# Performance work log

Hardware: AMD Instinct MI355X
Metric: run time of the kernel (lower is better)

The kernel has to match this reference:

```python
import jax, jax.numpy as jnp
import numpy as np

N = 262144          # number of samples
D = 512             # embedding dim
NUM_IDS = 8192      # label vocabulary size (fixed segment count for jit)


def setup_inputs() -> dict:
    key = jax.random.key(0)
    k_emb, k_lab = jax.random.split(key)
    emb = jax.random.normal(k_emb, (N, D), dtype=jnp.float32)
    labels = jax.random.randint(k_lab, (N,), 0, NUM_IDS, dtype=jnp.int64)
    return {"emb": emb, "labels": labels}


def reference(emb, labels):
    # torch.unique(labels, return_inverse=True); fixed size for jit.
    uniq_ids, inv = jnp.unique(labels, return_inverse=True, size=NUM_IDS, fill_value=-1)
    # scatter_add_ of rows grouped by inverse index -> segmented sum
    summed = jax.ops.segment_sum(emb, inv, num_segments=NUM_IDS)   # [NUM_IDS, D]
    # bincount(inv, minlength=num_ids)
    counts = jnp.bincount(inv, length=NUM_IDS)                      # [NUM_IDS]
    agg = summed / jnp.maximum(counts, 1).astype(emb.dtype)[:, None]
    return (agg, uniq_ids)
```

## Files before the change

### kernel.cpp

```cpp
#include <hip/hip_runtime.h>

#define NUM_IDS 8192
#define D 512


__global__ __launch_bounds__(256) void k_zero(int* __restrict__ cnt, int* __restrict__ cursor) {
    int i = blockIdx.x * 256 + threadIdx.x;
    if (i < NUM_IDS) { cnt[i] = 0; cursor[i] = 0; }
}

__global__ __launch_bounds__(256) void k_count(const int* __restrict__ labels, int n,
                                               int* __restrict__ cnt) {
    int i = blockIdx.x * 256 + threadIdx.x;
    if (i < n) atomicAdd(&cnt[labels[i]], 1);
}

__global__ __launch_bounds__(1024) void k_scan(const int* __restrict__ cnt,
                                               int* __restrict__ rank,
                                               int* __restrict__ offs,
                                               int* __restrict__ nuniq,
                                               float* __restrict__ uniq_out) {
    __shared__ int s_f[16], s_c[16];
    __shared__ int s_total;
    int t = threadIdx.x;
    int lane = t & 63, wave = t >> 6;
    int c[8], f[8];
    int fs = 0, cs = 0;
    int base = t * 8;
#pragma unroll
    for (int j = 0; j < 8; ++j) {
        c[j] = cnt[base + j];
        f[j] = (c[j] > 0) ? 1 : 0;
        fs += f[j]; cs += c[j];
    }
    int fi = fs, ci = cs;
#pragma unroll
    for (int d = 1; d < 64; d <<= 1) {
        int fo = __shfl_up(fi, d, 64);
        int co = __shfl_up(ci, d, 64);
        if (lane >= d) { fi += fo; ci += co; }
    }
    if (lane == 63) { s_f[wave] = fi; s_c[wave] = ci; }
    __syncthreads();
    if (t == 0) {
        int af = 0, ac = 0;
#pragma unroll
        for (int w = 0; w < 16; ++w) {
            int tf = s_f[w], tc = s_c[w];
            s_f[w] = af; s_c[w] = ac;
            af += tf; ac += tc;
        }
        s_total = af;
        nuniq[0] = af;
    }
    __syncthreads();
    int fexcl = (fi - fs) + s_f[wave];
    int cexcl = (ci - cs) + s_c[wave];
    int total = s_total;
#pragma unroll
    for (int j = 0; j < 8; ++j) {
        int id = base + j;
        rank[id] = fexcl;
        offs[id] = cexcl;
        if (f[j]) uniq_out[fexcl] = (float)id;
        if (id >= total) uniq_out[id] = -1.0f;
        fexcl += f[j];
        cexcl += c[j];
    }
}

__global__ __launch_bounds__(256) void k_fill(const int* __restrict__ labels, int n,
                                              const int* __restrict__ offs,
                                              int* __restrict__ cursor,
                                              int* __restrict__ rowidx) {
    int i = blockIdx.x * 256 + threadIdx.x;
    if (i < n) {
        int id = labels[i];
        int p = atomicAdd(&cursor[id], 1);
        rowidx[offs[id] + p] = i;
    }
}

__global__ __launch_bounds__(128) void k_agg(const float* __restrict__ emb,
                                             const int* __restrict__ cnt,
                                             const int* __restrict__ rank,
                                             const int* __restrict__ offs,
                                             const int* __restrict__ rowidx,
                                             const int* __restrict__ nuniq,
                                             float* __restrict__ agg) {
    int id = blockIdx.x;
    int t = threadIdx.x;
    int n = cnt[id];
    if (n == 0) {
        int outrow = nuniq[0] + (id - rank[id]);
        float4 z = {0.f, 0.f, 0.f, 0.f};
        reinterpret_cast<float4*>(agg + (size_t)outrow * D)[t] = z;
        return;
    }
    int off = offs[id];
    float ax0 = 0.f, ay0 = 0.f, az0 = 0.f, aw0 = 0.f;
    float ax1 = 0.f, ay1 = 0.f, az1 = 0.f, aw1 = 0.f;
    int r = 0;
    for (; r + 2 <= n; r += 2) {
        int r0 = rowidx[off + r];
        int r1 = rowidx[off + r + 1];
        float4 v0 = reinterpret_cast<const float4*>(emb + (size_t)r0 * D)[t];
        float4 v1 = reinterpret_cast<const float4*>(emb + (size_t)r1 * D)[t];
        ax0 += v0.x; ay0 += v0.y; az0 += v0.z; aw0 += v0.w;
        ax1 += v1.x; ay1 += v1.y; az1 += v1.z; aw1 += v1.w;
    }
    if (r < n) {
        int r0 = rowidx[off + r];
        float4 v0 = reinterpret_cast<const float4*>(emb + (size_t)r0 * D)[t];
        ax0 += v0.x; ay0 += v0.y; az0 += v0.z; aw0 += v0.w;
    }
    float inv = 1.0f / (float)n;
    float4 o;
    o.x = (ax0 + ax1) * inv;
    o.y = (ay0 + ay1) * inv;
    o.z = (az0 + az1) * inv;
    o.w = (aw0 + aw1) * inv;
    reinterpret_cast<float4*>(agg + (size_t)rank[id] * D)[t] = o;
}


extern "C" void kernel_launch(void* const* d_in, const int* in_sizes, int n_in,
                              void* d_out, int out_size, void* d_ws, size_t ws_size,
                              hipStream_t stream) {
    const float* emb   = (const float*)d_in[0];
    const int* labels  = (const int*)d_in[1];
    const int n = in_sizes[1];

    float* agg  = (float*)d_out;
    float* uniq = agg + (size_t)NUM_IDS * D;

    int* ws     = (int*)d_ws;
    int* cnt    = ws;
    int* rank   = ws + NUM_IDS;
    int* offs   = ws + 2 * NUM_IDS;
    int* cursor = ws + 3 * NUM_IDS;
    int* nuniq  = ws + 4 * NUM_IDS;
    int* rowidx = ws + 4 * NUM_IDS + 64;

    k_zero <<<NUM_IDS / 256, 256, 0, stream>>>(cnt, cursor);
    k_count<<<(n + 255) / 256, 256, 0, stream>>>(labels, n, cnt);
    k_scan <<<1, 1024, 0, stream>>>(cnt, rank, offs, nuniq, uniq);
    k_fill <<<(n + 255) / 256, 256, 0, stream>>>(labels, n, offs, cursor, rowidx);
    k_agg  <<<NUM_IDS, 128, 0, stream>>>(emb, cnt, rank, offs, rowidx, nuniq, agg);
}
```

Before: 155.3 us.

## Fuse count and scan via last-block ticket, preload cursor offsets, unroll aggregation

Merges the label counting and the prefix scan into one kernel. The last block to finish, detected through an atomic ticket, performs the scan with 256 threads over 32 ids each. Zeroing moves to a memset, and the cursor is seeded with the segment offsets so the fill step needs one atomic and no offs lookup. The aggregation loop is unrolled to four rows in flight per iteration. This removes two kernel launches and the serial single-block scan launch, in exchange for a grid-wide fence and a smaller scan block.

```diff
diff --git a/kernel.cpp b/kernel.cpp
--- a/kernel.cpp
+++ b/kernel.cpp
@@ -4,34 +4,39 @@
 #define D 512
 
 
-__global__ __launch_bounds__(256) void k_zero(int* __restrict__ cnt, int* __restrict__ cursor) {
-    int i = blockIdx.x * 256 + threadIdx.x;
-    if (i < NUM_IDS) { cnt[i] = 0; cursor[i] = 0; }
-}
+__global__ __launch_bounds__(256) void k_count_scan(
+    const int* __restrict__ labels, int n,
+    int* __restrict__ cnt,
+    int* __restrict__ rank,
+    int* __restrict__ offs,
+    int* __restrict__ cursor,
+    int* __restrict__ nuniq,
+    float* __restrict__ uniq_out)
+{
+    int tid = blockIdx.x * 256 + threadIdx.x;
+    int stride = gridDim.x * 256;
+    for (int i = tid; i < n; i += stride)
+        atomicAdd(&cnt[labels[i]], 1);
 
-__global__ __launch_bounds__(256) void k_count(const int* __restrict__ labels, int n,
-                                               int* __restrict__ cnt) {
-    int i = blockIdx.x * 256 + threadIdx.x;
-    if (i < n) atomicAdd(&cnt[labels[i]], 1);
-}
+    __threadfence();
+    __shared__ int s_last;
+    if (threadIdx.x == 0) {
+        int ticket = __hip_atomic_fetch_add(&cnt[NUM_IDS], 1,
+                                            __ATOMIC_ACQ_REL, __HIP_MEMORY_SCOPE_AGENT);
+        s_last = (ticket == (int)gridDim.x - 1) ? 1 : 0;
+    }
+    __syncthreads();
+    if (!s_last) return;
 
-__global__ __launch_bounds__(1024) void k_scan(const int* __restrict__ cnt,
-                                               int* __restrict__ rank,
-                                               int* __restrict__ offs,
-                                               int* __restrict__ nuniq,
-                                               float* __restrict__ uniq_out) {
-    __shared__ int s_f[16], s_c[16];
-    __shared__ int s_total;
     int t = threadIdx.x;
     int lane = t & 63, wave = t >> 6;
-    int c[8], f[8];
+    int base = t * 32;
+
     int fs = 0, cs = 0;
-    int base = t * 8;
 #pragma unroll
-    for (int j = 0; j < 8; ++j) {
-        c[j] = cnt[base + j];
-        f[j] = (c[j] > 0) ? 1 : 0;
-        fs += f[j]; cs += c[j];
+    for (int j = 0; j < 32; ++j) {
+        int c = __hip_atomic_load(&cnt[base + j], __ATOMIC_RELAXED, __HIP_MEMORY_SCOPE_AGENT);
+        fs += (c > 0); cs += c;
     }
     int fi = fs, ci = cs;
 #pragma unroll
@@ -40,12 +45,13 @@
         int co = __shfl_up(ci, d, 64);
         if (lane >= d) { fi += fo; ci += co; }
     }
+    __shared__ int s_f[4], s_c[4], s_total;
     if (lane == 63) { s_f[wave] = fi; s_c[wave] = ci; }
     __syncthreads();
     if (t == 0) {
         int af = 0, ac = 0;
 #pragma unroll
-        for (int w = 0; w < 16; ++w) {
+        for (int w = 0; w < 4; ++w) {
             int tf = s_f[w], tc = s_c[w];
             s_f[w] = af; s_c[w] = ac;
             af += tf; ac += tc;
@@ -58,26 +64,26 @@
     int cexcl = (ci - cs) + s_c[wave];
     int total = s_total;
 #pragma unroll
-    for (int j = 0; j < 8; ++j) {
+    for (int j = 0; j < 32; ++j) {
         int id = base + j;
+        int c = __hip_atomic_load(&cnt[id], __ATOMIC_RELAXED, __HIP_MEMORY_SCOPE_AGENT);
         rank[id] = fexcl;
         offs[id] = cexcl;
-        if (f[j]) uniq_out[fexcl] = (float)id;
+        cursor[id] = cexcl;
+        if (c > 0) uniq_out[fexcl] = (float)id;
         if (id >= total) uniq_out[id] = -1.0f;
-        fexcl += f[j];
-        cexcl += c[j];
+        fexcl += (c > 0);
+        cexcl += c;
     }
 }
 
 __global__ __launch_bounds__(256) void k_fill(const int* __restrict__ labels, int n,
-                                              const int* __restrict__ offs,
                                               int* __restrict__ cursor,
                                               int* __restrict__ rowidx) {
     int i = blockIdx.x * 256 + threadIdx.x;
     if (i < n) {
-        int id = labels[i];
-        int p = atomicAdd(&cursor[id], 1);
-        rowidx[offs[id] + p] = i;
+        int p = atomicAdd(&cursor[labels[i]], 1);
+        rowidx[p] = i;
     }
 }
 
@@ -91,6 +97,8 @@
     int id = blockIdx.x;
     int t = threadIdx.x;
     int n = cnt[id];
+    const float4* eb = reinterpret_cast<const float4*>(emb);
+
     if (n == 0) {
         int outrow = nuniq[0] + (id - rank[id]);
         float4 z = {0.f, 0.f, 0.f, 0.f};
@@ -98,28 +106,33 @@
         return;
     }
     int off = offs[id];
-    float ax0 = 0.f, ay0 = 0.f, az0 = 0.f, aw0 = 0.f;
-    float ax1 = 0.f, ay1 = 0.f, az1 = 0.f, aw1 = 0.f;
+    float4 a0 = {0,0,0,0}, a1 = {0,0,0,0}, a2 = {0,0,0,0}, a3 = {0,0,0,0};
     int r = 0;
-    for (; r + 2 <= n; r += 2) {
+    for (; r + 4 <= n; r += 4) {
+        int r0 = rowidx[off + r + 0];
+        int r1 = rowidx[off + r + 1];
+        int r2 = rowidx[off + r + 2];
+        int r3 = rowidx[off + r + 3];
+        float4 v0 = eb[(size_t)r0 * (D / 4) + t];
+        float4 v1 = eb[(size_t)r1 * (D / 4) + t];
+        float4 v2 = eb[(size_t)r2 * (D / 4) + t];
+        float4 v3 = eb[(size_t)r3 * (D / 4) + t];
+        a0.x += v0.x; a0.y += v0.y; a0.z += v0.z; a0.w += v0.w;
+        a1.x += v1.x; a1.y += v1.y; a1.z += v1.z; a1.w += v1.w;
+        a2.x += v2.x; a2.y += v2.y; a2.z += v2.z; a2.w += v2.w;
+        a3.x += v3.x; a3.y += v3.y; a3.z += v3.z; a3.w += v3.w;
+    }
+    for (; r < n; ++r) {
         int r0 = rowidx[off + r];
-        int r1 = rowidx[off + r + 1];
-        float4 v0 = reinterpret_cast<const float4*>(emb + (size_t)r0 * D)[t];
-        float4 v1 = reinterpret_cast<const float4*>(emb + (size_t)r1 * D)[t];
-        ax0 += v0.x; ay0 += v0.y; az0 += v0.z; aw0 += v0.w;
-        ax1 += v1.x; ay1 += v1.y; az1 += v1.z; aw1 += v1.w;
-    }
-    if (r < n) {
-        int r0 = rowidx[off + r];
-        float4 v0 = reinterpret_cast<const float4*>(emb + (size_t)r0 * D)[t];
-        ax0 += v0.x; ay0 += v0.y; az0 += v0.z; aw0 += v0.w;
+        float4 v0 = eb[(size_t)r0 * (D / 4) + t];
+        a0.x += v0.x; a0.y += v0.y; a0.z += v0.z; a0.w += v0.w;
     }
     float inv = 1.0f / (float)n;
     float4 o;
-    o.x = (ax0 + ax1) * inv;
-    o.y = (ay0 + ay1) * inv;
-    o.z = (az0 + az1) * inv;
-    o.w = (aw0 + aw1) * inv;
+    o.x = ((a0.x + a1.x) + (a2.x + a3.x)) * inv;
+    o.y = ((a0.y + a1.y) + (a2.y + a3.y)) * inv;
+    o.z = ((a0.z + a1.z) + (a2.z + a3.z)) * inv;
+    o.w = ((a0.w + a1.w) + (a2.w + a3.w)) * inv;
     reinterpret_cast<float4*>(agg + (size_t)rank[id] * D)[t] = o;
 }
 
@@ -136,15 +149,15 @@
 
     int* ws     = (int*)d_ws;
     int* cnt    = ws;
-    int* rank   = ws + NUM_IDS;
-    int* offs   = ws + 2 * NUM_IDS;
-    int* cursor = ws + 3 * NUM_IDS;
-    int* nuniq  = ws + 4 * NUM_IDS;
-    int* rowidx = ws + 4 * NUM_IDS + 64;
+    int* rank   = ws + NUM_IDS + 64;
+    int* offs   = rank + NUM_IDS;
+    int* cursor = offs + NUM_IDS;
+    int* nuniq  = cursor + NUM_IDS;
+    int* rowidx = nuniq + 64;
 
-    k_zero <<<NUM_IDS / 256, 256, 0, stream>>>(cnt, cursor);
-    k_count<<<(n + 255) / 256, 256, 0, stream>>>(labels, n, cnt);
-    k_scan <<<1, 1024, 0, stream>>>(cnt, rank, offs, nuniq, uniq);
-    k_fill <<<(n + 255) / 256, 256, 0, stream>>>(labels, n, offs, cursor, rowidx);
-    k_agg  <<<NUM_IDS, 128, 0, stream>>>(emb, cnt, rank, offs, rowidx, nuniq, agg);
+    hipMemsetAsync(cnt, 0, (NUM_IDS + 64) * sizeof(int), stream);
+
+    k_count_scan<<<1024, 256, 0, stream>>>(labels, n, cnt, rank, offs, cursor, nuniq, uniq);
+    k_fill      <<<(n + 255) / 256, 256, 0, stream>>>(labels, n, cursor, rowidx);
+    k_agg       <<<NUM_IDS, 128, 0, stream>>>(emb, cnt, rank, offs, rowidx, nuniq, agg);
 }
```

Result: slower. 242.0 us (+55.8%).
